# Kernel tuning notes

Hardware: AMD Instinct MI355X
Metric: run time of the kernel (lower is better)

Reference implementation:

```python
import jax, jax.numpy as jnp
from jax import lax
import numpy as np

N_SEGMENT = 8
N_DIV = 4
C = 256
NT = 64  # n_batch(8) * n_segment(8)
H = W = 56


def _ms_weights(planes, n_div):
    fold = planes // n_div
    w1 = np.zeros((planes, 1, 1, 1, 1), np.float32); w1[:, 0, 0] = 1.0
    w3 = np.zeros((planes, 1, 3, 1, 1), np.float32)
    w3[:fold, 0, 0] = 1.0; w3[fold:2 * fold, 0, 2] = 1.0; w3[2 * fold:, 0, 1] = 1.0
    w5 = np.zeros((planes, 1, 5, 1, 1), np.float32)
    w5[:fold, 0, :2] = 1.0; w5[fold:2 * fold, 0, 3:] = 1.0; w5[2 * fold:, 0, 2] = 1.0
    w7 = np.zeros((planes, 1, 7, 1, 1), np.float32)
    w7[:fold, 0, :3] = 1.0; w7[fold:2 * fold, 0, 4:] = 1.0; w7[2 * fold:, 0, 3] = 1.0
    return w1, w3, w5, w7


def setup_inputs() -> dict:
    key = jax.random.key(0)
    kx, kn = jax.random.split(key)
    x = jax.random.normal(kx, (NT, C, H, W), dtype=jnp.float32)
    w1, w3, w5, w7 = _ms_weights(C // 4, N_DIV)
    net_w = jax.random.normal(kn, (C, C, 1, 1), dtype=jnp.float32) * (1.0 / np.sqrt(C))
    return {
        "x": x,
        "w1": jnp.asarray(w1), "w3": jnp.asarray(w3),
        "w5": jnp.asarray(w5), "w7": jnp.asarray(w7),
        "net_w": net_w,
    }


def _dw_temporal_conv3d(x, w, pad):
    # x: (n, c4, T, h, w); w: (c4, 1, K, 1, 1) depthwise over temporal dim
    return lax.conv_general_dilated(
        x, w, window_strides=(1, 1, 1),
        padding=[(pad, pad), (0, 0), (0, 0)],
        dimension_numbers=("NCDHW", "OIDHW", "NCDHW"),
        feature_group_count=x.shape[1])


def reference(x, w1, w3, w5, w7, net_w):
    nt, c, h, wd = x.shape
    n = nt // N_SEGMENT
    c4 = c // 4
    # (nt,c,h,w) -> (n, c, T, h, w)
    xv = x.reshape(n, N_SEGMENT, c, h, wd).transpose(0, 2, 1, 3, 4)
    ws = (w1, w3, w5, w7)
    pads = (0, 1, 2, 3)
    ys = [_dw_temporal_conv3d(xv[:, i * c4:(i + 1) * c4], ws[i], pads[i])
          for i in range(4)]
    y = jnp.concatenate(ys, axis=1)                       # (n, c, T, h, w)
    y = y.transpose(0, 2, 1, 3, 4).reshape(nt, c, h, wd)  # back to (nt,c,h,w)
    # wrapped net: bias-free 1x1 Conv2d
    out = lax.conv_general_dilated(
        y, net_w, window_strides=(1, 1), padding="VALID",
        dimension_numbers=("NCHW", "OIHW", "NCHW"))
    return out
```

## Files before the change

kernel.cpp:

```cpp
#include <hip/hip_runtime.h>

#define HW 3136
#define C_ 256
#define T_ 8
#define NPOS 64
#define NBLK_PER_NT 49
#define YSTRIDE 40
#define KP 352
#define NKS 11
#define FLAGBIT 0x40000000

typedef __attribute__((ext_vector_type(8))) short bf16x8;
typedef __attribute__((ext_vector_type(4))) float f32x4;
typedef __attribute__((ext_vector_type(4))) unsigned int u32x4;
typedef __attribute__((ext_vector_type(4))) int i32x4;

__device__ __forceinline__ unsigned short f2bf(float f) {
  unsigned int u = __float_as_uint(f);
  u += 0x7FFF + ((u >> 16) & 1);
  return (unsigned short)(u >> 16);
}


__global__ void prep_table(const float* __restrict__ w1, const float* __restrict__ w3,
                           const float* __restrict__ w5, const float* __restrict__ w7,
                           int* __restrict__ slotC, float* __restrict__ slotW,
                           int* __restrict__ rowtab) {
  const int c = threadIdx.x;
  for (int s = c; s < KP; s += 256) {
    slotC[s] = 0;
    slotW[s] = 0.f;
    for (int t = 0; t < T_; ++t) rowtab[t * KP + s] = 0;
  }
  const int g = c >> 6, lc = c & 63, K = 2 * g + 1;
  const float* wsrc = (g == 0) ? w1 : (g == 1) ? w3 : (g == 2) ? w5 : w7;
  float w[3] = {0.f, 0.f, 0.f};
  int d[3] = {0, 0, 0};
  int cnt = 0;
  for (int k = 0; k < K && cnt < 3; ++k) {
    float v = wsrc[lc * K + k];
    if (v != 0.0f) { w[cnt] = v; d[cnt] = k - g; ++cnt; }
  }
  __shared__ int ps[256];
  ps[c] = cnt;
  __syncthreads();
  for (int dlt = 1; dlt < 256; dlt <<= 1) {
    int v = (c >= dlt) ? ps[c - dlt] : 0;
    __syncthreads();
    ps[c] += v;
    __syncthreads();
  }
  const int off = ps[c] - cnt;
  for (int i = 0; i < cnt; ++i) {
    const int s = off + i;
    if (s >= KP) break;
    slotC[s] = c;
    slotW[s] = w[i];
    for (int t = 0; t < T_; ++t) {
      const int tq = t + d[i];
      const bool valid = (unsigned)tq < (unsigned)T_;
      const int tqc = valid ? tq : (tq < 0 ? 0 : T_ - 1);
      rowtab[t * KP + s] = ((tqc * C_ + c) * HW) | (valid ? 0 : FLAGBIT);
    }
  }
}

__global__ void prep_wb(const float* __restrict__ net_w, const int* __restrict__ slotC,
                        const float* __restrict__ slotW, unsigned short* __restrict__ Wbp) {
  const int oc = blockIdx.x;
  const int s = threadIdx.x;
  if (s < KP) Wbp[oc * KP + s] = f2bf(net_w[oc * C_ + slotC[s]] * slotW[s]);
}

__global__ __launch_bounds__(256, 3) void fused_kernel(
    const float* __restrict__ x, const unsigned short* __restrict__ Wbp,
    const int* __restrict__ rowtab, float* __restrict__ out) {
  const int blk = blockIdx.x;
  const int nt = blk / NBLK_PER_NT;
  const int p0 = (blk % NBLK_PER_NT) * NPOS;
  const int n = nt >> 3, t = nt & 7;
  const int tid = threadIdx.x;
  const int lane = tid & 63;
  const int wv = tid >> 6;
  const int m16 = lane & 15;
  const int quad = lane >> 4;
  const int pp = tid & 63;
  const int chunk = tid >> 6;

  __shared__ __align__(16) unsigned short ylds[2][NPOS * YSTRIDE];
  __shared__ __align__(16) int ltab[KP];

  for (int i = tid; i < KP; i += 256) ltab[i] = rowtab[t * KP + i];

  f32x4 acc[4][4];
#pragma unroll
  for (int i = 0; i < 4; ++i)
#pragma unroll
    for (int j = 0; j < 4; ++j) acc[i][j] = (f32x4){0.f, 0.f, 0.f, 0.f};

  const float* xn = x + (size_t)(n * 8) * C_ * HW + (size_t)(p0 + pp);

  __syncthreads();

#define LOADX(KS, DST)                                          \
  do {                                                          \
    const i32x4 o0 = *(const i32x4*)&ltab[(KS) * 32 + chunk * 8];      \
    const i32x4 o1 = *(const i32x4*)&ltab[(KS) * 32 + chunk * 8 + 4];  \
    _Pragma("unroll") for (int j = 0; j < 4; ++j) {             \
      const int ofa = o0[j];                                    \
      const float va = xn[ofa & (FLAGBIT - 1)];                 \
      (DST)[j] = (ofa & FLAGBIT) ? 0.f : va;                    \
      const int ofb = o1[j];                                    \
      const float vb = xn[ofb & (FLAGBIT - 1)];                 \
      (DST)[4 + j] = (ofb & FLAGBIT) ? 0.f : vb;                \
    }                                                           \
  } while (0)

  float xv[3][8];
  LOADX(0, xv[0]);
  LOADX(1, xv[1]);

#pragma unroll
  for (int ks = 0; ks < NKS; ++ks) {
    const int cur = ks % 3;
    const int nxt = (ks + 2) % 3;
    const int buf = ks & 1;
    bf16x8 af[4];
#pragma unroll
    for (int mi = 0; mi < 4; ++mi)
      af[mi] = *(const bf16x8*)&Wbp[(size_t)((wv * 64 + mi * 16 + m16) * KP) + ks * 32 + quad * 8];
    unsigned short pk[8];
#pragma unroll
    for (int j = 0; j < 8; ++j) pk[j] = f2bf(xv[cur][j]);
    *(u32x4*)&ylds[buf][pp * YSTRIDE + chunk * 8] = *(const u32x4*)pk;
    if (ks + 2 < NKS) LOADX(ks + 2, xv[nxt]);
    __builtin_amdgcn_sched_barrier(0);
    asm volatile("s_waitcnt lgkmcnt(0)" ::: "memory");
    __builtin_amdgcn_s_barrier();
    __builtin_amdgcn_sched_barrier(0);
#pragma unroll
    for (int ni = 0; ni < 4; ++ni) {
      const bf16x8 bfrag = *(const bf16x8*)&ylds[buf][(ni * 16 + m16) * YSTRIDE + quad * 8];
#pragma unroll
      for (int mi = 0; mi < 4; ++mi)
        acc[mi][ni] =
            __builtin_amdgcn_mfma_f32_16x16x32_bf16(af[mi], bfrag, acc[mi][ni], 0, 0, 0);
    }
  }
#undef LOADX

  const size_t obase = (size_t)nt * C_ * HW + p0 + m16;
#pragma unroll
  for (int mi = 0; mi < 4; ++mi) {
#pragma unroll
    for (int r = 0; r < 4; ++r) {
      const int oc = wv * 64 + mi * 16 + quad * 4 + r;
      float* orow = out + obase + (size_t)oc * HW;
#pragma unroll
      for (int ni = 0; ni < 4; ++ni) orow[ni * 16] = acc[mi][ni][r];
    }
  }
}

extern "C" void kernel_launch(void* const* d_in, const int* in_sizes, int n_in,
                              void* d_out, int out_size, void* d_ws, size_t ws_size,
                              hipStream_t stream) {
  const float* x = (const float*)d_in[0];
  const float* w1 = (const float*)d_in[1];
  const float* w3 = (const float*)d_in[2];
  const float* w5 = (const float*)d_in[3];
  const float* w7 = (const float*)d_in[4];
  const float* net_w = (const float*)d_in[5];
  float* out = (float*)d_out;

  char* ws = (char*)d_ws;
  unsigned short* Wbp = (unsigned short*)ws;
  int* slotC = (int*)(ws + 180224);
  float* slotW = (float*)(ws + 181632);
  int* rowtab = (int*)(ws + 183040);

  hipLaunchKernelGGL(prep_table, dim3(1), dim3(256), 0, stream, w1, w3, w5, w7,
                     slotC, slotW, rowtab);
  hipLaunchKernelGGL(prep_wb, dim3(C_), dim3(384), 0, stream, net_w, slotC, slotW, Wbp);
  hipLaunchKernelGGL(fused_kernel, dim3(64 * NBLK_PER_NT), dim3(256), 0, stream,
                     x, Wbp, rowtab, out);
}
```

Baseline: 396.4 us.

## Deepen software pipeline: prefetch weights and x three stages ahead, issue MFMAs before packing

Restructures the K-loop so each iteration first runs the MFMAs on the already-packed LDS tile, then packs the next tile, prefetches weight fragments two steps ahead (double-buffered registers), and loads x three steps ahead. Out-of-range masking moves from a per-load select to a bitmask applied during bf16 packing. The aim is to hide global load latency for both A and B operands behind the matrix work. In exchange it raises register pressure, which could hurt occupancy at 3 blocks per SM.

```diff
diff --git a/kernel.cpp b/kernel.cpp
--- a/kernel.cpp
+++ b/kernel.cpp
@@ -99,55 +99,82 @@
     for (int j = 0; j < 4; ++j) acc[i][j] = (f32x4){0.f, 0.f, 0.f, 0.f};
 
   const float* xn = x + (size_t)(n * 8) * C_ * HW + (size_t)(p0 + pp);
+  const unsigned short* wbpp = Wbp + (wv * 64 + m16) * KP + quad * 8;
 
   __syncthreads();
 
-#define LOADX(KS, DST)                                          \
-  do {                                                          \
-    const i32x4 o0 = *(const i32x4*)&ltab[(KS) * 32 + chunk * 8];      \
-    const i32x4 o1 = *(const i32x4*)&ltab[(KS) * 32 + chunk * 8 + 4];  \
-    _Pragma("unroll") for (int j = 0; j < 4; ++j) {             \
-      const int ofa = o0[j];                                    \
-      const float va = xn[ofa & (FLAGBIT - 1)];                 \
-      (DST)[j] = (ofa & FLAGBIT) ? 0.f : va;                    \
-      const int ofb = o1[j];                                    \
-      const float vb = xn[ofb & (FLAGBIT - 1)];                 \
-      (DST)[4 + j] = (ofb & FLAGBIT) ? 0.f : vb;                \
-    }                                                           \
+#define LOADX(KS, DST, FM)                                              \
+  do {                                                                  \
+    const i32x4 o0 = *(const i32x4*)&ltab[(KS) * 32 + chunk * 8];       \
+    const i32x4 o1 = *(const i32x4*)&ltab[(KS) * 32 + chunk * 8 + 4];   \
+    int fm_ = 0;                                                        \
+    _Pragma("unroll") for (int j = 0; j < 4; ++j) {                     \
+      (DST)[j] = xn[o0[j] & (FLAGBIT - 1)];                             \
+      (DST)[4 + j] = xn[o1[j] & (FLAGBIT - 1)];                         \
+      fm_ |= ((o0[j] >> 30) & 1) << j;                                  \
+      fm_ |= ((o1[j] >> 30) & 1) << (4 + j);                            \
+    }                                                                   \
+    (FM) = fm_;                                                         \
+  } while (0)
+
+#define PACK(SRC, FM, BUF)                                                     \
+  do {                                                                         \
+    unsigned short pk[8];                                                      \
+    _Pragma("unroll") for (int j = 0; j < 8; ++j) {                            \
+      const unsigned short msk = (unsigned short)((((FM) >> j) & 1u) - 1u);    \
+      pk[j] = (unsigned short)(f2bf((SRC)[j]) & msk);                          \
+    }                                                                          \
+    *(u32x4*)&ylds[BUF][pp * YSTRIDE + chunk * 8] = *(const u32x4*)pk;         \
+  } while (0)
+
+#define LOADAF(KS, SLOT)                                                \
+  do {                                                                  \
+    _Pragma("unroll") for (int mi = 0; mi < 4; ++mi)                    \
+      afr[SLOT][mi] = *(const bf16x8*)&wbpp[mi * 16 * KP + (KS) * 32];  \
+  } while (0)
+
+#define KBARRIER()                                       \
+  do {                                                   \
+    __builtin_amdgcn_sched_barrier(0);                   \
+    asm volatile("s_waitcnt lgkmcnt(0)" ::: "memory");   \
+    __builtin_amdgcn_s_barrier();                        \
+    __builtin_amdgcn_sched_barrier(0);                   \
   } while (0)
 
   float xv[3][8];
-  LOADX(0, xv[0]);
-  LOADX(1, xv[1]);
+  int fm[3];
+  bf16x8 afr[2][4];
+  LOADX(0, xv[0], fm[0]);
+  LOADAF(0, 0);
+  LOADX(1, xv[1], fm[1]);
+  PACK(xv[0], fm[0], 0);
+  LOADAF(1, 1);
+  LOADX(2, xv[2], fm[2]);
+  KBARRIER();
 
 #pragma unroll
   for (int ks = 0; ks < NKS; ++ks) {
-    const int cur = ks % 3;
-    const int nxt = (ks + 2) % 3;
     const int buf = ks & 1;
-    bf16x8 af[4];
-#pragma unroll
-    for (int mi = 0; mi < 4; ++mi)
-      af[mi] = *(const bf16x8*)&Wbp[(size_t)((wv * 64 + mi * 16 + m16) * KP) + ks * 32 + quad * 8];
-    unsigned short pk[8];
-#pragma unroll
-    for (int j = 0; j < 8; ++j) pk[j] = f2bf(xv[cur][j]);
-    *(u32x4*)&ylds[buf][pp * YSTRIDE + chunk * 8] = *(const u32x4*)pk;
-    if (ks + 2 < NKS) LOADX(ks + 2, xv[nxt]);
-    __builtin_amdgcn_sched_barrier(0);
-    asm volatile("s_waitcnt lgkmcnt(0)" ::: "memory");
-    __builtin_amdgcn_s_barrier();
-    __builtin_amdgcn_sched_barrier(0);
 #pragma unroll
     for (int ni = 0; ni < 4; ++ni) {
       const bf16x8 bfrag = *(const bf16x8*)&ylds[buf][(ni * 16 + m16) * YSTRIDE + quad * 8];
 #pragma unroll
       for (int mi = 0; mi < 4; ++mi)
-        acc[mi][ni] =
-            __builtin_amdgcn_mfma_f32_16x16x32_bf16(af[mi], bfrag, acc[mi][ni], 0, 0, 0);
+        acc[mi][ni] = __builtin_amdgcn_mfma_f32_16x16x32_bf16(afr[ks & 1][mi], bfrag,
+                                                              acc[mi][ni], 0, 0, 0);
+    }
+    __builtin_amdgcn_sched_barrier(0);
+    if (ks + 1 < NKS) {
+      PACK(xv[(ks + 1) % 3], fm[(ks + 1) % 3], buf ^ 1);
+      if (ks + 2 < NKS) LOADAF(ks + 2, ks & 1);
+      if (ks + 3 < NKS) LOADX(ks + 3, xv[ks % 3], fm[ks % 3]);
+      KBARRIER();
     }
   }
 #undef LOADX
+#undef PACK
+#undef LOADAF
+#undef KBARRIER
 
   const size_t obase = (size_t)nt * C_ * HW + p0 + m16;
 #pragma unroll
```

Result: no change. 403.0 us (+1.7%).

## Load x directly into MFMA B-fragments, drop LDS staging and barriers

Applied to the files above, without the earlier changes.

The fused kernel now uses 512 threads per block and splits the 64 positions into two halves of 32, with four waves covering output channels. Each lane gathers its own x values straight into registers in the MFMA B-operand layout, masks out-of-range taps with a bitmask, and packs them to bf16 without going through shared memory. This removes the per-k-step LDS write, the s_barrier and the LDS fragment reads, and prefetches weight fragments one step ahead. In exchange, each x element is loaded redundantly by the four channel-group waves (relying on cache), and the per-lane loads become strided 16-element gathers rather than one coalesced position per thread.

```diff
diff --git a/kernel.cpp b/kernel.cpp
--- a/kernel.cpp
+++ b/kernel.cpp
@@ -5,7 +5,6 @@
 #define T_ 8
 #define NPOS 64
 #define NBLK_PER_NT 49
-#define YSTRIDE 40
 #define KP 352
 #define NKS 11
 #define FLAGBIT 0x40000000
@@ -15,10 +14,9 @@
 typedef __attribute__((ext_vector_type(4))) unsigned int u32x4;
 typedef __attribute__((ext_vector_type(4))) int i32x4;
 
-__device__ __forceinline__ unsigned short f2bf(float f) {
+__device__ __forceinline__ unsigned int f2bf_u(float f) {
   unsigned int u = __float_as_uint(f);
-  u += 0x7FFF + ((u >> 16) & 1);
-  return (unsigned short)(u >> 16);
+  return (u + 0x7FFFu + ((u >> 16) & 1u)) >> 16;
 }
 
 
@@ -69,10 +67,10 @@
                         const float* __restrict__ slotW, unsigned short* __restrict__ Wbp) {
   const int oc = blockIdx.x;
   const int s = threadIdx.x;
-  if (s < KP) Wbp[oc * KP + s] = f2bf(net_w[oc * C_ + slotC[s]] * slotW[s]);
-}
-
-__global__ __launch_bounds__(256, 3) void fused_kernel(
+  if (s < KP) Wbp[oc * KP + s] = (unsigned short)f2bf_u(net_w[oc * C_ + slotC[s]] * slotW[s]);
+}
+
+__global__ __launch_bounds__(512, 4) void fused_kernel(
     const float* __restrict__ x, const unsigned short* __restrict__ Wbp,
     const int* __restrict__ rowtab, float* __restrict__ out) {
   const int blk = blockIdx.x;
@@ -84,80 +82,96 @@
   const int wv = tid >> 6;
   const int m16 = lane & 15;
   const int quad = lane >> 4;
-  const int pp = tid & 63;
-  const int chunk = tid >> 6;
-
-  __shared__ __align__(16) unsigned short ylds[2][NPOS * YSTRIDE];
+  const int ocq = wv & 3;
+  const int ph = wv >> 2;
+
   __shared__ __align__(16) int ltab[KP];
-
-  for (int i = tid; i < KP; i += 256) ltab[i] = rowtab[t * KP + i];
-
-  f32x4 acc[4][4];
+  for (int i = tid; i < KP; i += 512) ltab[i] = rowtab[t * KP + i];
+
+  f32x4 acc[4][2];
 #pragma unroll
   for (int i = 0; i < 4; ++i)
 #pragma unroll
-    for (int j = 0; j < 4; ++j) acc[i][j] = (f32x4){0.f, 0.f, 0.f, 0.f};
-
-  const float* xn = x + (size_t)(n * 8) * C_ * HW + (size_t)(p0 + pp);
+    for (int j = 0; j < 2; ++j) acc[i][j] = (f32x4){0.f, 0.f, 0.f, 0.f};
+
+  const float* xpos = x + (size_t)(n * 8) * C_ * HW + (size_t)(p0 + ph * 32 + m16);
+  const unsigned short* wb = Wbp + (ocq * 64 + m16) * KP + quad * 8;
 
   __syncthreads();
 
-#define LOADX(KS, DST)                                          \
-  do {                                                          \
-    const i32x4 o0 = *(const i32x4*)&ltab[(KS) * 32 + chunk * 8];      \
-    const i32x4 o1 = *(const i32x4*)&ltab[(KS) * 32 + chunk * 8 + 4];  \
-    _Pragma("unroll") for (int j = 0; j < 4; ++j) {             \
-      const int ofa = o0[j];                                    \
-      const float va = xn[ofa & (FLAGBIT - 1)];                 \
-      (DST)[j] = (ofa & FLAGBIT) ? 0.f : va;                    \
-      const int ofb = o1[j];                                    \
-      const float vb = xn[ofb & (FLAGBIT - 1)];                 \
-      (DST)[4 + j] = (ofb & FLAGBIT) ? 0.f : vb;                \
-    }                                                           \
+#define LOADX(KS, P)                                                   \
+  do {                                                                 \
+    const i32x4 ro0 = *(const i32x4*)&ltab[(KS) * 32 + quad * 8];      \
+    const i32x4 ro1 = *(const i32x4*)&ltab[(KS) * 32 + quad * 8 + 4];  \
+    int fm_ = 0;                                                       \
+    _Pragma("unroll") for (int j = 0; j < 4; ++j) {                    \
+      const float* rpa = xpos + (ro0[j] & (FLAGBIT - 1));              \
+      const float* rpb = xpos + (ro1[j] & (FLAGBIT - 1));              \
+      _Pragma("unroll") for (int ni = 0; ni < 2; ++ni) {               \
+        xv[P][j][ni] = rpa[ni * 16];                                   \
+        xv[P][4 + j][ni] = rpb[ni * 16];                               \
+      }                                                                \
+      fm_ |= ((ro0[j] >> 30) & 1) << j;                                \
+      fm_ |= ((ro1[j] >> 30) & 1) << (4 + j);                          \
+    }                                                                  \
+    fm[P] = fm_;                                                       \
   } while (0)
 
-  float xv[3][8];
-  LOADX(0, xv[0]);
-  LOADX(1, xv[1]);
+#define LOADAF(KS)                                                     \
+  do {                                                                 \
+    _Pragma("unroll") for (int mi = 0; mi < 4; ++mi)                   \
+      afr[mi] = *(const bf16x8*)&wb[mi * 16 * KP + (KS) * 32];         \
+  } while (0)
+
+#define PACKMFMA(P)                                                    \
+  do {                                                                 \
+    unsigned int msk[8];                                               \
+    _Pragma("unroll") for (int j = 0; j < 8; ++j)                      \
+      msk[j] = ((unsigned int)((fm[P] >> j) & 1)) - 1u;                \
+    _Pragma("unroll") for (int ni = 0; ni < 2; ++ni) {                 \
+      u32x4 bd;                                                        \
+      _Pragma("unroll") for (int d2 = 0; d2 < 4; ++d2) {               \
+        const unsigned int lo =                                        \
+            f2bf_u(__uint_as_float(__float_as_uint(xv[P][2 * d2][ni]) & msk[2 * d2]));  \
+        const unsigned int hi =                                        \
+            f2bf_u(__uint_as_float(__float_as_uint(xv[P][2 * d2 + 1][ni]) & msk[2 * d2 + 1])); \
+        bd[d2] = (lo & 0xFFFFu) | (hi << 16);                          \
+      }                                                                \
+      const bf16x8 bfrag = *(const bf16x8*)&bd;                        \
+      _Pragma("unroll") for (int mi = 0; mi < 4; ++mi)                 \
+        acc[mi][ni] = __builtin_amdgcn_mfma_f32_16x16x32_bf16(afr[mi], bfrag, \
+                                                              acc[mi][ni], 0, 0, 0); \
+    }                                                                  \
+  } while (0)
+
+  float xv[2][8][2];
+  int fm[2];
+  bf16x8 afr[4];
+
+  LOADX(0, 0);
+  LOADAF(0);
 
 #pragma unroll
   for (int ks = 0; ks < NKS; ++ks) {
-    const int cur = ks % 3;
-    const int nxt = (ks + 2) % 3;
-    const int buf = ks & 1;
-    bf16x8 af[4];
-#pragma unroll
-    for (int mi = 0; mi < 4; ++mi)
-      af[mi] = *(const bf16x8*)&Wbp[(size_t)((wv * 64 + mi * 16 + m16) * KP) + ks * 32 + quad * 8];
-    unsigned short pk[8];
-#pragma unroll
-    for (int j = 0; j < 8; ++j) pk[j] = f2bf(xv[cur][j]);
-    *(u32x4*)&ylds[buf][pp * YSTRIDE + chunk * 8] = *(const u32x4*)pk;
-    if (ks + 2 < NKS) LOADX(ks + 2, xv[nxt]);
+    if (ks + 1 < NKS) LOADX(ks + 1, (ks + 1) & 1);
     __builtin_amdgcn_sched_barrier(0);
-    asm volatile("s_waitcnt lgkmcnt(0)" ::: "memory");
-    __builtin_amdgcn_s_barrier();
+    PACKMFMA(ks & 1);
+    if (ks + 1 < NKS) LOADAF(ks + 1);
     __builtin_amdgcn_sched_barrier(0);
-#pragma unroll
-    for (int ni = 0; ni < 4; ++ni) {
-      const bf16x8 bfrag = *(const bf16x8*)&ylds[buf][(ni * 16 + m16) * YSTRIDE + quad * 8];
-#pragma unroll
-      for (int mi = 0; mi < 4; ++mi)
-        acc[mi][ni] =
-            __builtin_amdgcn_mfma_f32_16x16x32_bf16(af[mi], bfrag, acc[mi][ni], 0, 0, 0);
-    }
   }
 #undef LOADX
-
-  const size_t obase = (size_t)nt * C_ * HW + p0 + m16;
+#undef LOADAF
+#undef PACKMFMA
+
+  const size_t obase = (size_t)nt * C_ * HW + p0 + ph * 32 + m16;
 #pragma unroll
   for (int mi = 0; mi < 4; ++mi) {
 #pragma unroll
     for (int r = 0; r < 4; ++r) {
-      const int oc = wv * 64 + mi * 16 + quad * 4 + r;
+      const int oc = ocq * 64 + mi * 16 + quad * 4 + r;
       float* orow = out + obase + (size_t)oc * HW;
 #pragma unroll
-      for (int ni = 0; ni < 4; ++ni) orow[ni * 16] = acc[mi][ni][r];
+      for (int ni = 0; ni < 2; ++ni) orow[ni * 16] = acc[mi][ni][r];
     }
   }
 }
@@ -182,6 +196,6 @@
   hipLaunchKernelGGL(prep_table, dim3(1), dim3(256), 0, stream, w1, w3, w5, w7,
                      slotC, slotW, rowtab);
   hipLaunchKernelGGL(prep_wb, dim3(C_), dim3(384), 0, stream, net_w, slotC, slotW, Wbp);
-  hipLaunchKernelGGL(fused_kernel, dim3(64 * NBLK_PER_NT), dim3(256), 0, stream,
+  hipLaunchKernelGGL(fused_kernel, dim3(64 * NBLK_PER_NT), dim3(512), 0, stream,
                      x, Wbp, rowtab, out);
 }
```

Result: slower. 486.2 us (+22.6%).
